# Performance work log

Measured on AMD Instinct MI355X. Metric: run time of the kernel, lower is better.

The kernel has to match this reference:

```python
import jax, jax.numpy as jnp
import numpy as np

DIM = 2048
N_HEADS = 16
N_KV_HEADS = 4
HEAD_DIM = DIM // N_HEADS  # 128
ROPE_BASE = 10000.0
B, S = 4, 2048


def rope_tables(seq_len, head_dim, base, dtype):
    half = head_dim // 2
    inv_freq = 1.0 / (base ** (jnp.arange(0, head_dim, 2, dtype=jnp.float32) / head_dim))
    t = jnp.arange(seq_len, dtype=jnp.float32)
    freqs = jnp.outer(t, inv_freq)  # [S, half]
    return jnp.cos(freqs).astype(dtype), jnp.sin(freqs).astype(dtype)


def apply_rotary(x, cos, sin):
    # x: [B, H, S, D]; cos/sin: [S, D/2] broadcast over B,H
    half = x.shape[-1] // 2
    x1, x2 = x[..., :half], x[..., half:]
    return jnp.concatenate((x1 * cos + x2 * sin, x1 * -sin + x2 * cos), axis=-1)


def setup_inputs() -> dict:
    key = jax.random.key(0)
    ks = jax.random.split(key, 5)
    sc = 1.0 / np.sqrt(DIM)
    return {
        "x": jax.random.normal(ks[0], (B, S, DIM), dtype=jnp.float32),
        "wq": jax.random.normal(ks[1], (DIM, DIM), dtype=jnp.float32) * sc,
        "wk": jax.random.normal(ks[2], (N_KV_HEADS * HEAD_DIM, DIM), dtype=jnp.float32) * sc,
        "wv": jax.random.normal(ks[3], (N_KV_HEADS * HEAD_DIM, DIM), dtype=jnp.float32) * sc,
        "wo": jax.random.normal(ks[4], (DIM, DIM), dtype=jnp.float32) * sc,
    }


def reference(x, wq, wk, wv, wo):
    bsz, seqlen, _ = x.shape
    q = jnp.einsum("bsd,ed->bse", x, wq).reshape(bsz, seqlen, N_HEADS, HEAD_DIM).transpose(0, 2, 1, 3)
    k = jnp.einsum("bsd,ed->bse", x, wk).reshape(bsz, seqlen, N_KV_HEADS, HEAD_DIM).transpose(0, 2, 1, 3)
    v = jnp.einsum("bsd,ed->bse", x, wv).reshape(bsz, seqlen, N_KV_HEADS, HEAD_DIM).transpose(0, 2, 1, 3)

    cos, sin = rope_tables(seqlen, HEAD_DIM, ROPE_BASE, q.dtype)
    q = apply_rotary(q, cos, sin)
    k = apply_rotary(k, cos, sin)

    rep = N_HEADS // N_KV_HEADS
    if rep > 1:
        k = jnp.repeat(k, rep, axis=1)
        v = jnp.repeat(v, rep, axis=1)

    scale = 1.0 / np.sqrt(HEAD_DIM)
    logits = jnp.einsum("bhqd,bhkd->bhqk", q, k) * scale
    causal = jnp.tril(jnp.ones((seqlen, seqlen), dtype=bool))
    logits = jnp.where(causal, logits, jnp.finfo(logits.dtype).min)
    attn = jax.nn.softmax(logits, axis=-1)
    y = jnp.einsum("bhqk,bhkd->bhqd", attn, v)

    y = y.transpose(0, 2, 1, 3).reshape(bsz, seqlen, DIM)
    return jnp.einsum("bsd,ed->bse", y, wo)
```

## Files before the change

### kernel.cpp

```cpp
#include <hip/hip_runtime.h>
#include <hip/hip_bf16.h>

typedef short s16x8 __attribute__((ext_vector_type(8)));
typedef float f32x4 __attribute__((ext_vector_type(4)));
typedef float f32x16 __attribute__((ext_vector_type(16)));
typedef unsigned u32;
typedef unsigned u32x4 __attribute__((ext_vector_type(4)));
typedef unsigned short u16;

#define DMODEL 2048
#define NH     16
#define NKV    4
#define HD     128
#define NB     4
#define SS     2048

static __device__ __forceinline__ u16 f2bf(float f) {
  unsigned u = __builtin_bit_cast(unsigned, f);
  u += 0x7fffu + ((u >> 16) & 1u);
  return (u16)(u >> 16);
}
static __device__ __forceinline__ float bf2f(u16 h) {
  unsigned u = ((unsigned)h) << 16;
  return __builtin_bit_cast(float, u);
}
static __device__ __forceinline__ u32 packbf(float a, float b) {
  return (u32)f2bf(a) | ((u32)f2bf(b) << 16);
}

typedef const __attribute__((address_space(1))) void* gas_p;
typedef __attribute__((address_space(3))) void* las_p;
#define GLOAD16(g, l) __builtin_amdgcn_global_load_lds((gas_p)(const void*)(g), (las_p)(void*)(l), 16, 0, 0)

__global__ void cast_all(const float* __restrict__ x,  const float* __restrict__ wq,
                         const float* __restrict__ wk, const float* __restrict__ wv,
                         const float* __restrict__ wo,
                         u16* __restrict__ xb, u16* __restrict__ wqkv, u16* __restrict__ wob)
{
  long gid = (long)blockIdx.x * 256 + threadIdx.x;
  long i = gid * 4;
  const float* src; u16* dst; long off;
  if (i < 16777216L)       { src = x;  dst = xb;             off = i; }
  else if (i < 20971520L)  { src = wq; dst = wqkv;           off = i - 16777216L; }
  else if (i < 22020096L)  { src = wk; dst = wqkv + 4194304; off = i - 20971520L; }
  else if (i < 23068672L)  { src = wv; dst = wqkv + 5242880; off = i - 22020096L; }
  else                     { src = wo; dst = wob;            off = i - 23068672L; }
  float4 v = *(const float4*)(src + off);
  ushort4 o;
  o.x = f2bf(v.x); o.y = f2bf(v.y); o.z = f2bf(v.z); o.w = f2bf(v.w);
  *(ushort4*)(dst + off) = o;
}

#define GPHASE(MQ, STG, WAIT)                                               \
  {                                                                         \
    s16x8 af[2][2];                                                         \
    _Pragma("unroll") for (int j = 0; j < 2; j++)                           \
      _Pragma("unroll") for (int ks = 0; ks < 2; ks++) {                    \
        int rr = (MQ) * 32 + j * 16 + lr;                                   \
        int c = ks * 4 + lg;                                                \
        af[j][ks] = *(const s16x8*)(ab + rr * 128 + ((c ^ (rr & 7)) * 16)); \
      }                                                                     \
    STG;                                                                    \
    WAIT;                                                                   \
    asm volatile("" ::: "memory");                                          \
    __builtin_amdgcn_s_barrier();                                           \
    asm volatile("" ::: "memory");                                          \
    __builtin_amdgcn_s_setprio(1);                                          \
    _Pragma("unroll") for (int ks = 0; ks < 2; ks++)                        \
      _Pragma("unroll") for (int j = 0; j < 2; j++)                         \
        _Pragma("unroll") for (int n = 0; n < 4; n++)                       \
          acc[(MQ) * 2 + j][n] = __builtin_amdgcn_mfma_f32_16x16x32_bf16(   \
              af[j][ks], bfr[n][ks], acc[(MQ) * 2 + j][n], 0, 0, 0);        \
    __builtin_amdgcn_s_setprio(0);                                          \
    asm volatile("" ::: "memory");                                          \
    __builtin_amdgcn_s_barrier();                                           \
    asm volatile("" ::: "memory");                                          \
  }

template<int NT, int EPI>
__global__ __launch_bounds__(512) void gemm256(
    const u16* __restrict__ A, const u16* __restrict__ Bm, int K,
    u16* __restrict__ Oq, u16* __restrict__ Ok, u16* __restrict__ Ov, float* __restrict__ Of)
{
  __shared__ __align__(16) u16 lds[2][32768];
  const int tid = threadIdx.x, l = tid & 63, w = tid >> 6;
  const int lg = l >> 4, lr = l & 15;
  const int wm = w >> 2, wn = w & 3;

  const int nwg = NT * 32;
  const int cpx = nwg >> 3;
  const int bid = blockIdx.x;
  const int swz = (bid & 7) * cpx + (bid >> 3);
  const int by = swz / NT, bx = swz % NT;
  const int rowBase = by * 256, colBase = bx * 256;

  const int rloc = w * 8 + (l >> 3);
  const int cgo  = ((l & 7) ^ (l >> 3)) * 8;
  const u16* gp[8];
#pragma unroll
  for (int seg = 0; seg < 8; seg++) {
    int half = (seg >> 1) & 1;
    int row  = (seg & 1) * 64 + rloc;
    if (seg < 4) gp[seg] = A  + (long)(rowBase + half * 128 + row) * K + cgo;
    else         gp[seg] = Bm + (long)(colBase + half * 128 + row) * K + cgo;
  }

  f32x4 acc[8][4] = {};

  const int NKT = K >> 6;
  {
    char* nb = (char*)&lds[0][0];
#pragma unroll
    for (int seg = 0; seg < 8; seg++)
      GLOAD16(gp[seg], nb + seg * 8192 + w * 1024);
#pragma unroll
    for (int seg = 0; seg < 8; seg++) gp[seg] += 64;
    asm volatile("s_waitcnt vmcnt(0)" ::: "memory");
    __builtin_amdgcn_s_barrier();
    asm volatile("" ::: "memory");
  }

  for (int kt = 0; kt < NKT; kt++) {
    const int cur = kt & 1;
    const bool pre = (kt + 1 < NKT);
    const char* ab = (const char*)&lds[cur][0] + wm * 16384;
    const char* bb = (const char*)&lds[cur][0] + 32768 + (wn >> 1) * 16384;
    char* nb = (char*)&lds[cur ^ 1][0];
    const int rbB = (wn & 1) * 64;

    s16x8 bfr[4][2];
#pragma unroll
    for (int n = 0; n < 4; n++)
#pragma unroll
      for (int ks = 0; ks < 2; ks++) {
        int rb = rbB + n * 16 + lr;
        int c = ks * 4 + lg;
        bfr[n][ks] = *(const s16x8*)(bb + rb * 128 + ((c ^ (rb & 7)) * 16));
      }
    GPHASE(0,
      { if (pre) { GLOAD16(gp[4], nb + 4 * 8192 + w * 1024);
                   GLOAD16(gp[5], nb + 5 * 8192 + w * 1024); } },
      { });
    GPHASE(1,
      { if (pre) { GLOAD16(gp[6], nb + 6 * 8192 + w * 1024);
                   GLOAD16(gp[7], nb + 7 * 8192 + w * 1024); } },
      { if (pre) { asm volatile("s_waitcnt vmcnt(4)" ::: "memory"); }
        else     { asm volatile("s_waitcnt vmcnt(0)" ::: "memory"); } });
    GPHASE(2,
      { if (pre) { GLOAD16(gp[0], nb + 0 * 8192 + w * 1024);
                   GLOAD16(gp[2], nb + 2 * 8192 + w * 1024); } },
      { });
    GPHASE(3,
      { if (pre) { GLOAD16(gp[1], nb + 1 * 8192 + w * 1024);
                   GLOAD16(gp[3], nb + 3 * 8192 + w * 1024); } },
      { if (pre) { asm volatile("s_waitcnt vmcnt(2)" ::: "memory"); } });

    if (pre) {
#pragma unroll
      for (int seg = 0; seg < 8; seg++) gp[seg] += 64;
    }
  }

#pragma unroll
  for (int m = 0; m < 8; m++)
#pragma unroll
    for (int n = 0; n < 4; n++)
#pragma unroll
      for (int r = 0; r < 4; r++) {
        int row = rowBase + wm * 128 + m * 16 + lg * 4 + r;
        int col = colBase + wn * 64 + n * 16 + lr;
        float v = acc[m][n][r];
        if (EPI == 0) {
          int b = row >> 11, s = row & 2047;
          u16 hv = f2bf(v);
          if (col < 2048) {
            int hh = col >> 7, d = col & 127;
            Oq[(((long)(b * NH + hh)) * SS + s) * HD + d] = hv;
          } else if (col < 2560) {
            int c2 = col - 2048, kh = c2 >> 7, d = c2 & 127;
            Ok[(((long)(b * NKV + kh)) * SS + s) * HD + d] = hv;
          } else {
            int c2 = col - 2560, kh = c2 >> 7, d = c2 & 127;
            Ov[(((long)(b * NKV + kh)) * HD + d) * SS + s] = hv;
          }
        } else {
          Of[(long)row * DMODEL + col] = v;
        }
      }
}

__global__ void rope_kernel(u16* __restrict__ Qr, u16* __restrict__ Kr)
{
  long gid = (long)blockIdx.x * 256 + threadIdx.x;
  int i = (int)(gid & 63);
  long row = gid >> 6;
  int s;
  u16* p;
  const long qrows = (long)NB * NH * SS;
  if (row < qrows) { s = (int)(row & 2047); p = Qr + row * HD; }
  else             { long r2 = row - qrows; s = (int)(r2 & 2047); p = Kr + r2 * HD; }
  float inv = exp2f(-(float)i * 0.20762050593046015f);
  float fr = (float)s * inv;
  float c = cosf(fr), sn = sinf(fr);
  float x1 = bf2f(p[i]), x2 = bf2f(p[i + 64]);
  p[i]      = f2bf(x1 * c + x2 * sn);
  p[i + 64] = f2bf(-x1 * sn + x2 * c);
}

__global__ __launch_bounds__(512) void attn_fwd(const u16* __restrict__ Qr, const u16* __restrict__ Kr,
                                                const u16* __restrict__ Vt, u16* __restrict__ Y)
{
  __shared__ __align__(16) u16 Ks[2][64 * 128];
  __shared__ __align__(16) u16 Vs[2][128 * 64];

  const int tid = threadIdx.x, l = tid & 63, w = tid >> 6;
  const int lq = l & 31, hi = l >> 5;
  const int p = blockIdx.x, h = blockIdx.y, b = blockIdx.z;
  const int kvh = h >> 2;

  const u16* Kh = Kr + ((long)(b * NKV + kvh)) * SS * HD;
  const u16* Vh = Vt + ((long)(b * NKV + kvh)) * HD * SS;
  const float scale = 0.08838834764831845f;

  auto stageK = [&](int buf, int kvb) {
    char* kb = (char*)&Ks[buf][0];
#pragma unroll
    for (int i = 0; i < 2; i++) {
      int L = w * 2048 + i * 1024 + l * 16;
      int r = L >> 8;
      int cl = (L >> 4) & 15;
      int cg = (cl & 8) | ((cl ^ r) & 7);
      GLOAD16((const char*)(Kh + (long)(kvb + r) * HD) + cg * 16, kb + w * 2048 + i * 1024);
    }
  };
  auto stageV = [&](int buf, int kvb) {
    char* vb = (char*)&Vs[buf][0];
#pragma unroll
    for (int i = 0; i < 2; i++) {
      int L = w * 2048 + i * 1024 + l * 16;
      int r = L >> 7;
      int cl = (L >> 4) & 7;
      int cg = (cl ^ r) & 7;
      GLOAD16((const char*)(Vh + (long)r * SS + kvb) + cg * 16, vb + w * 2048 + i * 1024);
    }
  };

  for (int job = 0; job < 2; job++) {
    const int qt = job ? p : 7 - p;
    const int qRow0 = qt * 256 + w * 32;
    const int qMax = qRow0 + 31;
    const int nT = 4 * qt + 4;
    const int myq = qRow0 + lq;
    const u16* Qh = Qr + (((long)(b * NH + h)) * SS + qRow0) * HD;
    u16* Yh = Y + ((long)b * SS) * DMODEL + h * HD;

    s16x8 qf[8];
#pragma unroll
    for (int kk = 0; kk < 8; kk++)
      qf[kk] = *(const s16x8*)(Qh + (long)lq * HD + kk * 16 + hi * 8);

    float m_run = -1e30f, l_run = 0.f;
    f32x16 oacc[4] = {};

    stageK(0, 0); stageV(0, 0);

    for (int t = 0; t < nT; t++) {
      const int cur = t & 1;
      if (t + 1 < nT) {
        stageK(cur ^ 1, (t + 1) * 64);
        stageV(cur ^ 1, (t + 1) * 64);
        asm volatile("s_waitcnt vmcnt(4)" ::: "memory");
      } else {
        asm volatile("s_waitcnt vmcnt(0)" ::: "memory");
      }
      __builtin_amdgcn_s_barrier();
      asm volatile("" ::: "memory");

      if (t * 64 <= qMax) {
        const char* kb = (const char*)&Ks[cur][0];
        const char* vb = (const char*)&Vs[cur][0];
        f32x16 sacc[2] = {};
#pragma unroll
        for (int kk = 0; kk < 8; kk++) {
          int ch = kk * 2 + hi;
#pragma unroll
          for (int tile = 0; tile < 2; tile++) {
            int rr = tile * 32 + lq;
            int cs = (ch & 8) | ((ch ^ rr) & 7);
            s16x8 kf = *(const s16x8*)(kb + rr * 256 + cs * 16);
            sacc[tile] = __builtin_amdgcn_mfma_f32_32x32x16_bf16(kf, qf[kk], sacc[tile], 0, 0, 0);
          }
        }
        const bool full = (t * 64 + 63 <= qRow0);
        float pmax = -1e30f;
#pragma unroll
        for (int tile = 0; tile < 2; tile++)
#pragma unroll
          for (int r = 0; r < 16; r++) {
            int kv = t * 64 + tile * 32 + (r & 3) + 8 * (r >> 2) + 4 * hi;
            float v = sacc[tile][r] * scale;
            if (!full && kv > myq) v = -30000.f;
            sacc[tile][r] = v;
            pmax = fmaxf(pmax, v);
          }
        pmax = fmaxf(pmax, __shfl_xor(pmax, 32));
        if (!__all(pmax - m_run <= 8.0f)) {
          float mnew = fmaxf(m_run, pmax);
          float sf = __expf(m_run - mnew);
          m_run = mnew; l_run *= sf;
          int sfi = __builtin_bit_cast(int, sf);
#pragma unroll
          for (int r = 0; r < 16; r++) {
            int qq = (r & 3) + 8 * (r >> 2) + 4 * hi;
            float sfr = __builtin_bit_cast(float, __builtin_amdgcn_ds_bpermute(qq << 2, sfi));
#pragma unroll
            for (int n = 0; n < 4; n++) oacc[n][r] *= sfr;
          }
        }
        float rs = 0.f;
#pragma unroll
        for (int tile = 0; tile < 2; tile++)
#pragma unroll
          for (int r = 0; r < 16; r++) {
            float pv = __expf(sacc[tile][r] - m_run);
            sacc[tile][r] = pv;
            rs += pv;
          }
        rs += __shfl_xor(rs, 32);
        l_run += rs;
        s16x8 pav[4];
#pragma unroll
        for (int tile = 0; tile < 2; tile++) {
          u32 qk[8], sw[8];
#pragma unroll
          for (int j = 0; j < 8; j++) {
            qk[j] = packbf(sacc[tile][2 * j], sacc[tile][2 * j + 1]);
            sw[j] = __shfl_xor(qk[j], 32);
          }
          u32x4 f0, f1;
          f0[0] = hi ? sw[2] : qk[0];
          f0[1] = hi ? sw[3] : qk[1];
          f0[2] = hi ? qk[2] : sw[0];
          f0[3] = hi ? qk[3] : sw[1];
          f1[0] = hi ? sw[6] : qk[4];
          f1[1] = hi ? sw[7] : qk[5];
          f1[2] = hi ? qk[6] : sw[4];
          f1[3] = hi ? qk[7] : sw[5];
          pav[tile * 2 + 0] = __builtin_bit_cast(s16x8, f0);
          pav[tile * 2 + 1] = __builtin_bit_cast(s16x8, f1);
        }
#pragma unroll
        for (int n = 0; n < 4; n++) {
          int rr = n * 32 + lq;
#pragma unroll
          for (int kk = 0; kk < 4; kk++) {
            int ch = kk * 2 + hi;
            int cs = (ch ^ rr) & 7;
            s16x8 vf = *(const s16x8*)(vb + rr * 128 + cs * 16);
            oacc[n] = __builtin_amdgcn_mfma_f32_32x32x16_bf16(pav[kk], vf, oacc[n], 0, 0, 0);
          }
        }
      }
      asm volatile("" ::: "memory");
      __builtin_amdgcn_s_barrier();
      asm volatile("" ::: "memory");
    }

    float linv = 1.f / l_run;
    int li = __builtin_bit_cast(int, linv);
#pragma unroll
    for (int r = 0; r < 16; r++) {
      int qq = (r & 3) + 8 * (r >> 2) + 4 * hi;
      float lr_ = __builtin_bit_cast(float, __builtin_amdgcn_ds_bpermute(qq << 2, li));
      u16* yrow = Yh + (long)(qRow0 + qq) * DMODEL;
#pragma unroll
      for (int n = 0; n < 4; n++)
        yrow[n * 32 + lq] = f2bf(oacc[n][r] * lr_);
    }
  }
}

extern "C" void kernel_launch(void* const* d_in, const int* in_sizes, int n_in,
                              void* d_out, int out_size, void* d_ws, size_t ws_size,
                              hipStream_t stream) {
  const float* x  = (const float*)d_in[0];
  const float* wq = (const float*)d_in[1];
  const float* wk = (const float*)d_in[2];
  const float* wv = (const float*)d_in[3];
  const float* wo = (const float*)d_in[4];
  float* out = (float*)d_out;
  char* ws = (char*)d_ws;

  u16* Xb   = (u16*)ws;
  u16* Wqkv = (u16*)(ws + 33554432);
  u16* Wob  = (u16*)(ws + 46137344);
  u16* Qr   = (u16*)(ws + 54525952);
  u16* Kr   = (u16*)(ws + 88080384);
  u16* Vt   = (u16*)(ws + 96468992);
  u16* Y    = Xb;

  cast_all<<<26624, 256, 0, stream>>>(x, wq, wk, wv, wo, Xb, Wqkv, Wob);
  gemm256<12, 0><<<384, 512, 0, stream>>>(Xb, Wqkv, DMODEL, Qr, Kr, Vt, nullptr);
  rope_kernel<<<40960, 256, 0, stream>>>(Qr, Kr);
  dim3 ag(4, NH, NB);
  attn_fwd<<<ag, 512, 0, stream>>>(Qr, Kr, Vt, Y);
  gemm256<8, 1><<<256, 512, 0, stream>>>(Y, Wob, DMODEL, nullptr, nullptr, nullptr, out);
}
```

Measured before the change: 370.5 us.

## Use 128x256-tile double-buffered GEMM for the QKV projection

Adds a new gemm128 kernel with a 128-row by 256-column output tile and a simple two-buffer LDS pipeline, and uses it for the QKV projection instead of the 256x256 gemm256. The grid doubles from 384 to 768 workgroups, which should fill the CUs more evenly and reduce wave-quantization tail effects on the projection. In exchange, each tile reloads the B operand more often, and the simpler pipeline with a barrier every K step may overlap loads with MFMA less well than the phased gemm256. The epilogue is factored into a shared helper, and the output projection is unchanged.

```diff
diff --git a/kernel.cpp b/kernel.cpp
--- a/kernel.cpp
+++ b/kernel.cpp
@@ -49,6 +49,118 @@
   ushort4 o;
   o.x = f2bf(v.x); o.y = f2bf(v.y); o.z = f2bf(v.z); o.w = f2bf(v.w);
   *(ushort4*)(dst + off) = o;
+}
+
+static __device__ __forceinline__ void epi_store(int EPI, int row, int col, float v,
+    u16* __restrict__ Oq, u16* __restrict__ Ok, u16* __restrict__ Ov, float* __restrict__ Of)
+{
+  if (EPI == 0) {
+    int b = row >> 11, s = row & 2047;
+    u16 hv = f2bf(v);
+    if (col < 2048) {
+      int hh = col >> 7, d = col & 127;
+      Oq[(((long)(b * NH + hh)) * SS + s) * HD + d] = hv;
+    } else if (col < 2560) {
+      int c2 = col - 2048, kh = c2 >> 7, d = c2 & 127;
+      Ok[(((long)(b * NKV + kh)) * SS + s) * HD + d] = hv;
+    } else {
+      int c2 = col - 2560, kh = c2 >> 7, d = c2 & 127;
+      Ov[(((long)(b * NKV + kh)) * HD + d) * SS + s] = hv;
+    }
+  } else {
+    Of[(long)row * DMODEL + col] = v;
+  }
+}
+
+template<int NTC, int EPI>
+__global__ __launch_bounds__(512) void gemm128(
+    const u16* __restrict__ A, const u16* __restrict__ Bm, int K,
+    u16* __restrict__ Oq, u16* __restrict__ Ok, u16* __restrict__ Ov, float* __restrict__ Of)
+{
+  __shared__ __align__(16) u16 lds[2][24576];
+  const int tid = threadIdx.x, l = tid & 63, w = tid >> 6;
+  const int lg = l >> 4, lr = l & 15;
+  const int wm = w >> 2, wn = w & 3;
+
+  const int nwg = NTC * 64;
+  const int cpx = nwg >> 3;
+  const int bid = blockIdx.x;
+  const int swz = (bid & 7) * cpx + (bid >> 3);
+  const int by = swz / NTC, bx = swz % NTC;
+  const int rowBase = by * 128, colBase = bx * 256;
+
+  const int rloc = w * 8 + (l >> 3);
+  const int cgo  = ((l & 7) ^ (l >> 3)) * 8;
+  const u16* gp[6];
+#pragma unroll
+  for (int seg = 0; seg < 6; seg++) {
+    if (seg < 2) gp[seg] = A  + (long)(rowBase + seg * 64 + rloc) * K + cgo;
+    else         gp[seg] = Bm + (long)(colBase + (seg - 2) * 64 + rloc) * K + cgo;
+  }
+
+  f32x4 acc[4][4] = {};
+
+  auto stage = [&](int buf) {
+    char* base = (char*)&lds[buf][0];
+#pragma unroll
+    for (int seg = 0; seg < 6; seg++)
+      GLOAD16(gp[seg], base + seg * 8192 + w * 1024);
+  };
+
+  const int NKT = K >> 6;
+  stage(0);
+#pragma unroll
+  for (int seg = 0; seg < 6; seg++) gp[seg] += 64;
+  asm volatile("s_waitcnt vmcnt(0)" ::: "memory");
+  __builtin_amdgcn_s_barrier();
+
+  for (int kt = 0; kt < NKT; kt++) {
+    const int cur = kt & 1;
+    if (kt + 1 < NKT) {
+      stage(cur ^ 1);
+#pragma unroll
+      for (int seg = 0; seg < 6; seg++) gp[seg] += 64;
+      asm volatile("s_waitcnt vmcnt(6)" ::: "memory");
+    } else {
+      asm volatile("s_waitcnt vmcnt(0)" ::: "memory");
+    }
+    __builtin_amdgcn_s_barrier();
+    asm volatile("" ::: "memory");
+
+    const char* ab = (const char*)&lds[cur][0] + wm * 8192;
+    const char* bb = (const char*)&lds[cur][0] + (2 + wn) * 8192;
+    s16x8 af[4][2], bfr[4][2];
+#pragma unroll
+    for (int m = 0; m < 4; m++)
+#pragma unroll
+      for (int ks = 0; ks < 2; ks++) {
+        int rr = m * 16 + lr;
+        int c = ks * 4 + lg;
+        af[m][ks]  = *(const s16x8*)(ab + rr * 128 + ((c ^ (rr & 7)) * 16));
+        bfr[m][ks] = *(const s16x8*)(bb + rr * 128 + ((c ^ (rr & 7)) * 16));
+      }
+    __builtin_amdgcn_s_setprio(1);
+#pragma unroll
+    for (int ks = 0; ks < 2; ks++)
+#pragma unroll
+      for (int m = 0; m < 4; m++)
+#pragma unroll
+        for (int n = 0; n < 4; n++)
+          acc[m][n] = __builtin_amdgcn_mfma_f32_16x16x32_bf16(af[m][ks], bfr[n][ks], acc[m][n], 0, 0, 0);
+    __builtin_amdgcn_s_setprio(0);
+    asm volatile("" ::: "memory");
+    __builtin_amdgcn_s_barrier();
+    asm volatile("" ::: "memory");
+  }
+
+#pragma unroll
+  for (int m = 0; m < 4; m++)
+#pragma unroll
+    for (int n = 0; n < 4; n++)
+#pragma unroll
+      for (int r = 0; r < 4; r++)
+        epi_store(EPI, rowBase + wm * 64 + m * 16 + lg * 4 + r,
+                  colBase + wn * 64 + n * 16 + lr, acc[m][n][r], Oq, Ok, Ov, Of);
 }
 
 #define GPHASE(MQ, STG, WAIT)                                               \
@@ -166,27 +278,9 @@
 #pragma unroll
     for (int n = 0; n < 4; n++)
 #pragma unroll
-      for (int r = 0; r < 4; r++) {
-        int row = rowBase + wm * 128 + m * 16 + lg * 4 + r;
-        int col = colBase + wn * 64 + n * 16 + lr;
-        float v = acc[m][n][r];
-        if (EPI == 0) {
-          int b = row >> 11, s = row & 2047;
-          u16 hv = f2bf(v);
-          if (col < 2048) {
-            int hh = col >> 7, d = col & 127;
-            Oq[(((long)(b * NH + hh)) * SS + s) * HD + d] = hv;
-          } else if (col < 2560) {
-            int c2 = col - 2048, kh = c2 >> 7, d = c2 & 127;
-            Ok[(((long)(b * NKV + kh)) * SS + s) * HD + d] = hv;
-          } else {
-            int c2 = col - 2560, kh = c2 >> 7, d = c2 & 127;
-            Ov[(((long)(b * NKV + kh)) * HD + d) * SS + s] = hv;
-          }
-        } else {
-          Of[(long)row * DMODEL + col] = v;
-        }
-      }
+      for (int r = 0; r < 4; r++)
+        epi_store(EPI, rowBase + wm * 128 + m * 16 + lg * 4 + r,
+                  colBase + wn * 64 + n * 16 + lr, acc[m][n][r], Oq, Ok, Ov, Of);
 }
 
 __global__ void rope_kernel(u16* __restrict__ Qr, u16* __restrict__ Kr)
@@ -400,7 +494,7 @@
   u16* Y    = Xb;
 
   cast_all<<<26624, 256, 0, stream>>>(x, wq, wk, wv, wo, Xb, Wqkv, Wob);
-  gemm256<12, 0><<<384, 512, 0, stream>>>(Xb, Wqkv, DMODEL, Qr, Kr, Vt, nullptr);
+  gemm128<12, 0><<<768, 512, 0, stream>>>(Xb, Wqkv, DMODEL, Qr, Kr, Vt, nullptr);
   rope_kernel<<<40960, 256, 0, stream>>>(Qr, Kr);
   dim3 ag(4, NH, NB);
   attn_fwd<<<ag, 512, 0, stream>>>(Qr, Kr, Vt, Y);
```

After: 393.9 us. 1.06x slower.
